# Kernel optimization log

Measured on AMD Instinct MI355X. Metric: run time of the kernel, lower is better.

Reference implementation:

```python
import jax, jax.numpy as jnp
import numpy as np
from jax import lax

_SQ2 = np.sqrt(2.0)
_H2 = (np.array([[1.0, 1.0], [1.0, -1.0]]) / _SQ2).astype(np.complex64)
_BN_INV = 1.0 / np.sqrt(1.0 + 1e-5)  # eval-mode BN, running_mean=0, running_var=1

# wire 0 is the most-significant bit of the 4-qubit basis index (PennyLane convention)
def _cnot_perm(c, t):
    p = np.arange(16)
    for b in range(16):
        if (b >> (3 - c)) & 1:
            p[b] = b ^ (1 << (3 - t))
    return p

# CNOT(0,1) then CNOT(1,2) then CNOT(2,3) then CNOT(3,0); psi_out = psi_in[perm]
_p01, _p12, _p23, _p30 = _cnot_perm(0, 1), _cnot_perm(1, 2), _cnot_perm(2, 3), _cnot_perm(3, 0)
_PTOT = _p01[_p12[_p23[_p30]]]
# PauliZ expectation signs: (16 basis states, 4 wires)
_ZM = np.array([[1.0 - 2.0 * ((b >> (3 - w)) & 1) for w in range(4)] for b in range(16)], np.float32)


def _make_unitaries(w0, w1):
    """w0, w1: (C,2). Circuit: H^4 -> RY(w0[0],w0[1],w0[0],w0[1]) -> RZ(w1 same pattern) -> CNOT ring."""
    ty = jnp.stack([w0[:, 0], w0[:, 1], w0[:, 0], w0[:, 1]], axis=1)  # (C,4)
    tz = jnp.stack([w1[:, 0], w1[:, 1], w1[:, 0], w1[:, 1]], axis=1)
    c, s = jnp.cos(ty / 2), jnp.sin(ty / 2)
    ry = jnp.stack([jnp.stack([c, -s], -1), jnp.stack([s, c], -1)], -2).astype(jnp.complex64)  # (C,4,2,2)
    ph = jnp.exp(-0.5j * tz.astype(jnp.complex64))  # (C,4)
    zr = jnp.zeros_like(ph)
    rz = jnp.stack([jnp.stack([ph, zr], -1), jnp.stack([zr, jnp.conj(ph)], -1)], -2)  # (C,4,2,2)
    g = rz @ ry @ jnp.asarray(_H2)  # per-wire single-qubit gate, (C,4,2,2)
    U = g[:, 0]
    for w in range(1, 4):  # kron over wires 0..3
        d = U.shape[1]
        U = jnp.einsum('cij,ckl->cikjl', U, g[:, w]).reshape(U.shape[0], d * 2, d * 2)
    return U[:, _PTOT, :]  # fold the CNOT-ring permutation into U


def _conv_bn_relu(x, w, g, b):
    y = lax.conv_general_dilated(x, w, (1, 1), ((1, 1), (1, 1)),
                                 dimension_numbers=('NCHW', 'OIHW', 'NCHW'))
    y = y * (g * _BN_INV)[None, :, None, None] + b[None, :, None, None]
    return jax.nn.relu(y)


def _bn_relu(x, g, b):
    return jax.nn.relu(x * (g * _BN_INV)[None, :, None, None] + b[None, :, None, None])


def _maxpool2(x):
    return lax.reduce_window(x, -jnp.inf, lax.max, (1, 1, 2, 2), (1, 1, 2, 2), 'VALID')


def _quantum_stage(e4, q_w0, q_w1):
    B, C, H, W = e4.shape
    xp = jnp.pad(e4, ((0, 0), (0, 0), (1, 2), (1, 2)))  # F.pad(1,2,1,2)
    # 4x4 patches, stride 1, row-major (matches torch unfold->view ordering): (B,C,H,W,16)
    patches = jnp.stack([xp[:, :, i:i + H, j:j + W] for i in range(4) for j in range(4)], axis=-1)
    nrm = jnp.sqrt(jnp.sum(patches * patches, axis=-1, keepdims=True))
    psi0 = (patches / jnp.maximum(nrm, 1e-12)).astype(jnp.complex64)  # AmplitudeEmbedding(normalize=True)
    U = _make_unitaries(q_w0, q_w1)  # (C,16,16) complex
    psi = jnp.einsum('cij,bchwj->bchwi', U, psi0)
    probs = psi.real ** 2 + psi.imag ** 2
    ev = jnp.einsum('bchwi,iq->bchwq', probs, jnp.asarray(_ZM))  # <Z_w> per wire
    return (ev.mean(-1) + 1.0) / 2.0


def setup_inputs() -> dict:
    key = jax.random.key(0)
    ks = jax.random.split(key, 18)
    conv_w = lambda k, o, i: jax.random.normal(k, (o, i, 3, 3), jnp.float32) / np.sqrt(i * 9)
    gamma = lambda k, c: jax.random.uniform(k, (c,), jnp.float32, 0.75, 1.25)
    beta = lambda k, c: 0.1 * jax.random.normal(k, (c,), jnp.float32)
    return {
        'x': jax.random.normal(ks[0], (8, 1, 256, 256), jnp.float32),
        'w1': conv_w(ks[1], 32, 1), 'g1': gamma(ks[2], 32), 'b1': beta(ks[3], 32),
        'w2': conv_w(ks[4], 64, 32), 'g2': gamma(ks[5], 64), 'b2': beta(ks[6], 64),
        'w3': conv_w(ks[7], 128, 64), 'g3': gamma(ks[8], 128), 'b3': beta(ks[9], 128),
        'w4': conv_w(ks[10], 256, 128), 'g4': gamma(ks[11], 256), 'b4': beta(ks[12], 256),
        'q_w0': 0.5 * jax.random.normal(ks[13], (256, 2), jnp.float32),
        'q_w1': 0.5 * jax.random.normal(ks[14], (256, 2), jnp.float32),
        'g5': gamma(ks[15], 256), 'b5': beta(ks[16], 256),
    }


def reference(x, w1, g1, b1, w2, g2, b2, w3, g3, b3, w4, g4, b4, q_w0, q_w1, g5, b5):
    e1 = _conv_bn_relu(x, w1, g1, b1)                 # (8,32,256,256)
    e2 = _conv_bn_relu(_maxpool2(e1), w2, g2, b2)     # (8,64,128,128)
    e3 = _conv_bn_relu(_maxpool2(e2), w3, g3, b3)     # (8,128,64,64)
    e4 = _conv_bn_relu(_maxpool2(e3), w4, g4, b4)     # (8,256,32,32)
    q = _quantum_stage(e4, q_w0, q_w1)                # (8,256,32,32)
    out4 = _bn_relu(q, g5, b5)
    return (e1, e2, e3, out4)
```

## Files before the change

kernel.cpp:

```cpp
#include <hip/hip_runtime.h>
#include <cstdint>
#include <cstddef>

#define BN_INV 0.9999950000374997f

typedef __attribute__((ext_vector_type(8))) _Float16 h8v;
typedef __attribute__((ext_vector_type(4))) float f4v;
typedef __attribute__((ext_vector_type(2))) float f2v;

__device__ __forceinline__ void fsplit(float v, ushort& h, ushort& l) {
    _Float16 hh = (_Float16)v;
    _Float16 ll = (_Float16)(v - (float)hh);
    h = __builtin_bit_cast(ushort, hh);
    l = __builtin_bit_cast(ushort, ll);
}

__device__ __forceinline__ void repack_one(
    const float* __restrict__ w, ushort* __restrict__ dst, int CIN, int i)
{
    int ocf = i / (CIN * 9);
    int r = i % (CIN * 9);
    int ic = r / 9;
    int tap = r % 9;
    int ocg = ocf >> 6, oc = ocf & 63;
    int chunk = ic >> 5, q = (ic >> 3) & 3, j = ic & 7;
    int nch = CIN >> 5;
    ushort h, l;
    fsplit(w[i], h, l);
    size_t base = (size_t)((ocg * nch + chunk) * 2) * 18432
                + (size_t)tap * 2048 + q * 512 + oc * 8 + j;
    dst[base] = h;
    dst[base + 18432] = l;
}

__global__ __launch_bounds__(256) void prep_conv1_kernel(
    const float* __restrict__ w0, const float* __restrict__ w1,
    float* __restrict__ U,
    const float* __restrict__ w2, ushort* __restrict__ wb2,
    const float* __restrict__ w3, ushort* __restrict__ wb3,
    const float* __restrict__ w4, ushort* __restrict__ wb4,
    const float* __restrict__ x, const float* __restrict__ wt,
    const float* __restrict__ g, const float* __restrict__ be,
    float* __restrict__ out, ushort* __restrict__ pooled)
{
    __shared__ float s_in[6][132];

    int blk = blockIdx.x;
    int tid = threadIdx.x;

    if (blk >= 1024) {
        if (blk >= 1400)     { repack_one(w4, wb4, 128, (blk - 1400) * 256 + tid); return; }
        if (blk >= 1112)     { repack_one(w3, wb3,  64, (blk - 1112) * 256 + tid); return; }
        if (blk >= 1040)     { repack_one(w2, wb2,  32, (blk - 1040) * 256 + tid); return; }

        int idx = (blk - 1024) * 256 + tid;
        int c = idx >> 4, r = idx & 15;
        float gr[4][2][2], gi[4][2][2];
        const float inv_sq2 = 0.70710678118654752f;
#pragma unroll
        for (int w = 0; w < 4; ++w) {
            float ty = w0[c * 2 + (w & 1)];
            float tz = w1[c * 2 + (w & 1)];
            float cy = cosf(0.5f * ty), sy = sinf(0.5f * ty);
            float cz = cosf(0.5f * tz), sz = sinf(0.5f * tz);
            float r00 = (cy - sy) * inv_sq2, r01 = (cy + sy) * inv_sq2;
            float r10 = (cy + sy) * inv_sq2, r11 = (sy - cy) * inv_sq2;
            gr[w][0][0] = cz * r00; gi[w][0][0] = -sz * r00;
            gr[w][0][1] = cz * r01; gi[w][0][1] = -sz * r01;
            gr[w][1][0] = cz * r10; gi[w][1][0] =  sz * r10;
            gr[w][1][1] = cz * r11; gi[w][1][1] =  sz * r11;
        }
        const int PTOT[16] = {0,13,3,14,6,11,5,8,12,1,15,2,10,7,9,4};
        int rp = PTOT[r];
        float* Uo = U + (size_t)c * 512 + r * 32;
#pragma unroll
        for (int cc = 0; cc < 16; ++cc) {
            float pr = 1.f, pi = 0.f;
#pragma unroll
            for (int w = 0; w < 4; ++w) {
                int ib = (rp >> (3 - w)) & 1, jb = (cc >> (3 - w)) & 1;
                float ar = gr[w][ib][jb], ai = gi[w][ib][jb];
                float nr = pr * ar - pi * ai;
                float ni = pr * ai + pi * ar;
                pr = nr; pi = ni;
            }
            Uo[cc * 2 + 0] = pr;
            Uo[cc * 2 + 1] = pi;
        }
        return;
    }

    int b = blk >> 7;
    int rest = blk & 127;
    int ty0 = (rest >> 1) * 4;
    int tx0 = (rest & 1) * 128;

    for (int i = tid; i < 780; i += 256) {
        int yy = i / 130, xx = i % 130;
        int gy = ty0 + yy - 1, gx = tx0 + xx - 1;
        float v = 0.f;
        if (gy >= 0 && gy < 256 && gx >= 0 && gx < 256)
            v = x[(size_t)b * 65536 + gy * 256 + gx];
        s_in[yy][xx] = v;
    }
    __syncthreads();

    int w = tid >> 6;
    int lane = tid & 63;
    int xp = (w & 1) * 32 + (lane >> 1);
    int ylo = lane & 1;
    int y = (w >> 1) * 2 + ylo;
    int x0s = xp * 2;

    f2v t2[3][3];
#pragma unroll
    for (int i = 0; i < 3; ++i) {
        f2v a = *(const f2v*)&s_in[y + i][x0s];
        f2v bq = *(const f2v*)&s_in[y + i][x0s + 2];
        t2[i][0] = a;
        t2[i][1] = (f2v){a.y, bq.x};
        t2[i][2] = bq;
    }

    bool wr_pool = (ylo == 0);
    int pyp = (ty0 >> 1) + (w >> 1);
    int pxp = (tx0 >> 1) + xp;
    ushort* op = pooled + (((size_t)b * 128 + pyp) * 128 + pxp) * 64;
    size_t obase = ((size_t)b * 32) * 65536 + (size_t)(ty0 + y) * 256 + (tx0 + x0s);

#pragma unroll
    for (int k = 0; k < 4; ++k) {
        uint uhw[4], ulw[4];
#pragma unroll
        for (int j2 = 0; j2 < 4; ++j2) {
            const int oc0 = k * 8 + j2 * 2;
            const int oc1 = oc0 + 1;
            f2v s0 = {0.f, 0.f}, s1 = {0.f, 0.f};
#pragma unroll
            for (int i = 0; i < 3; ++i)
#pragma unroll
                for (int j = 0; j < 3; ++j) {
                    s0 += wt[oc0 * 9 + i * 3 + j] * t2[i][j];
                    s1 += wt[oc1 * 9 + i * 3 + j] * t2[i][j];
                }
            float gs0 = g[oc0] * BN_INV, be0 = be[oc0];
            float gs1 = g[oc1] * BN_INV, be1 = be[oc1];
            s0 = s0 * gs0 + (f2v){be0, be0};
            s1 = s1 * gs1 + (f2v){be1, be1};
            s0.x = fmaxf(s0.x, 0.f); s0.y = fmaxf(s0.y, 0.f);
            s1.x = fmaxf(s1.x, 0.f); s1.y = fmaxf(s1.y, 0.f);
            *(f2v*)(out + obase + (size_t)oc0 * 65536) = s0;
            *(f2v*)(out + obase + (size_t)oc1 * 65536) = s1;
            float p0 = fmaxf(s0.x, s0.y);
            float p1 = fmaxf(s1.x, s1.y);
            p0 = fmaxf(p0, __shfl_xor(p0, 1));
            p1 = fmaxf(p1, __shfl_xor(p1, 1));
            auto hh = __builtin_amdgcn_cvt_pkrtz(p0, p1);
            uhw[j2] = __builtin_bit_cast(uint, hh);
            float l0 = p0 - (float)hh.x;
            float l1 = p1 - (float)hh.y;
            auto ll = __builtin_amdgcn_cvt_pkrtz(l0, l1);
            ulw[j2] = __builtin_bit_cast(uint, ll);
        }
        if (wr_pool) {
            uint4 uh = {uhw[0], uhw[1], uhw[2], uhw[3]};
            uint4 ul = {ulw[0], ulw[1], ulw[2], ulw[3]};
            *(uint4*)(op + 8 * k) = uh;
            *(uint4*)(op + 32 + 8 * k) = ul;
        }
    }
}

template <int CIN, int COUT, int HW, bool POOL>
__global__ __launch_bounds__(512) void conv3x3_mfma_split(
    const ushort* __restrict__ in,
    const ushort* __restrict__ wb,
    const float* __restrict__ g, const float* __restrict__ be,
    float* __restrict__ out,
    ushort* __restrict__ pooled)
{
    constexpr int NCH = CIN / 32;
    constexpr int NTX = HW / 16;
    constexpr int NT = NTX * (HW / 8);
    constexpr int NOCG = COUT / 64;
    constexpr int PS = 72;
    constexpr int BUFSZ = 180 * PS;
    constexpr int NBUF = (NCH > 1) ? 2 : 1;

    __shared__ __align__(16) ushort s_in[NBUF * BUFSZ];

    constexpr int NWG = NT * NOCG * 8;
    int bid = blockIdx.x;
    bid = (bid & 7) * (NWG >> 3) + (bid >> 3);

    int tile = bid % NT;
    int rest = bid / NT;
    int ocg = rest % NOCG;
    int b = rest / NOCG;
    int x0 = (tile % NTX) * 16;
    int y0 = (tile / NTX) * 8;

    int tid = threadIdx.x;
    int wv = tid >> 6;
    int lane = tid & 63;
    int n = lane & 15;
    int q = lane >> 4;
    int oc_half = (wv & 1) * 32;
    int sg = wv >> 1;

    int ib[2];
#pragma unroll
    for (int f = 0; f < 2; ++f)
        ib[f] = ((sg * 2 + f) * 18 + n) * PS + q * 8;
    int iwa0 = q * 512 + (oc_half + n) * 8;
    int iwa1 = q * 512 + (oc_half + 16 + n) * 8;

    const ushort* inb = in + (size_t)b * HW * HW * 2 * CIN;

    f4v acc[2][2];
#pragma unroll
    for (int a = 0; a < 2; ++a)
#pragma unroll
        for (int f = 0; f < 2; ++f) acc[a][f] = (f4v){0.f, 0.f, 0.f, 0.f};

    auto elem_addr = [&](int i, int& ldsoff, const ushort*& gsrc) {
        int pos = i >> 4;
        int r2 = i & 15;
        int comp = r2 >> 3;
        int u = r2 & 7;
        int py = pos / 18, px = pos % 18;
        int gy = y0 - 1 + py, gx = x0 - 1 + px;
        ldsoff = pos * PS + comp * 32 + u * 4;
        gsrc = (gy >= 0 && gy < HW && gx >= 0 && gx < HW)
             ? inb + ((size_t)gy * HW + gx) * (2 * CIN) + comp * CIN + u * 4
             : nullptr;
    };

#define TAPS(T0, T1)                                                             \
    _Pragma("unroll")                                                            \
    for (int tap = T0; tap < T1; ++tap) {                                        \
        const int toff = ((tap / 3) * 18 + (tap % 3)) * PS;                      \
        const ushort* wt_ = wc + tap * 2048;                                     \
        h8v ah0 = *(const h8v*)(wt_ + iwa0);                                     \
        h8v ah1 = *(const h8v*)(wt_ + iwa1);                                     \
        h8v al0 = *(const h8v*)(wt_ + 18432 + iwa0);                             \
        h8v al1 = *(const h8v*)(wt_ + 18432 + iwa1);                             \
        h8v bh[2], bl[2];                                                        \
        _Pragma("unroll")                                                        \
        for (int f = 0; f < 2; ++f) {                                            \
            bh[f] = *(const h8v*)(&sb[toff + ib[f]]);                            \
            bl[f] = *(const h8v*)(&sb[toff + ib[f] + 32]);                       \
        }                                                                        \
        _Pragma("unroll")                                                        \
        for (int f = 0; f < 2; ++f) {                                            \
            acc[0][f] = __builtin_amdgcn_mfma_f32_16x16x32_f16(ah0, bh[f], acc[0][f], 0, 0, 0); \
            acc[1][f] = __builtin_amdgcn_mfma_f32_16x16x32_f16(ah1, bh[f], acc[1][f], 0, 0, 0); \
        }                                                                        \
        _Pragma("unroll")                                                        \
        for (int f = 0; f < 2; ++f) {                                            \
            acc[0][f] = __builtin_amdgcn_mfma_f32_16x16x32_f16(ah0, bl[f], acc[0][f], 0, 0, 0); \
            acc[1][f] = __builtin_amdgcn_mfma_f32_16x16x32_f16(ah1, bl[f], acc[1][f], 0, 0, 0); \
        }                                                                        \
        _Pragma("unroll")                                                        \
        for (int f = 0; f < 2; ++f) {                                            \
            acc[0][f] = __builtin_amdgcn_mfma_f32_16x16x32_f16(al0, bh[f], acc[0][f], 0, 0, 0); \
            acc[1][f] = __builtin_amdgcn_mfma_f32_16x16x32_f16(al1, bh[f], acc[1][f], 0, 0, 0); \
        }                                                                        \
    }

    if constexpr (NCH == 1) {
#pragma unroll
        for (int it = 0; it < 5; ++it) {
            int i = tid + it * 512;
            if (i < 2304) {
                int lo; const ushort* src;
                elem_addr(i, lo, src);
                uint2 v; v.x = 0u; v.y = 0u;
                if (src) v = *(const uint2*)src;
                *(uint2*)(&s_in[lo]) = v;
            }
        }
        int lo0, lo1 = 0; const ushort* src0; const ushort* src1 = nullptr;
        elem_addr(2304 + tid, lo0, src0);
        bool has1 = tid < 64;
        if (has1) elem_addr(2816 + tid, lo1, src1);
        uint2 v0; v0.x = 0u; v0.y = 0u;
        uint2 v1; v1.x = 0u; v1.y = 0u;
        if (src0) v0 = *(const uint2*)src0;
        if (src1) v1 = *(const uint2*)src1;
        __syncthreads();

        const ushort* wc = wb + (size_t)(ocg * 2) * 18432;
        const ushort* sb = &s_in[0];
        __builtin_amdgcn_s_setprio(1);
        TAPS(0, 3)
        __builtin_amdgcn_s_setprio(0);
        *(uint2*)(&s_in[lo0]) = v0;
        if (has1) *(uint2*)(&s_in[lo1]) = v1;
        __syncthreads();
        __builtin_amdgcn_s_setprio(1);
        TAPS(3, 9)
        __builtin_amdgcn_s_setprio(0);
    } else {
        auto stage = [&](int ch, int bsel) {
#pragma unroll
            for (int it = 0; it < 6; ++it) {
                int i = tid + it * 512;
                if (i < 2880) {
                    int lo; const ushort* src;
                    elem_addr(i, lo, src);
                    uint2 v; v.x = 0u; v.y = 0u;
                    if (src) v = *(const uint2*)(src + (size_t)ch * 32);
                    *(uint2*)(&s_in[bsel * BUFSZ + lo]) = v;
                }
            }
        };

        stage(0, 0);
        int cur = 0;
        for (int ch = 0; ch < NCH; ++ch) {
            __syncthreads();
            if (ch + 1 < NCH) stage(ch + 1, cur ^ 1);

            const ushort* wc = wb + (size_t)((ocg * NCH + ch) * 2) * 18432;
            const ushort* sb = &s_in[cur * BUFSZ];
            __builtin_amdgcn_s_setprio(1);
            TAPS(0, 9)
            __builtin_amdgcn_s_setprio(0);
            cur ^= 1;
        }
    }
#undef TAPS

    float vr[2][2][4];
#pragma unroll
    for (int tf = 0; tf < 2; ++tf)
#pragma unroll
        for (int f = 0; f < 2; ++f) {
            int y = y0 + sg * 2 + f;
#pragma unroll
            for (int r = 0; r < 4; ++r) {
                int oc = ocg * 64 + oc_half + tf * 16 + q * 4 + r;
                float v = fmaxf(acc[tf][f][r] * (g[oc] * BN_INV) + be[oc], 0.f);
                vr[tf][f][r] = v;
                out[((size_t)(b * COUT + oc) * HW + y) * HW + (x0 + n)] = v;
            }
        }

    if (POOL) {
#pragma unroll
        for (int tf = 0; tf < 2; ++tf) {
            ushort h[4], l[4];
#pragma unroll
            for (int r = 0; r < 4; ++r) {
                float p = fmaxf(vr[tf][0][r], vr[tf][1][r]);
                p = fmaxf(p, __shfl_xor(p, 1));
                fsplit(p, h[r], l[r]);
            }
            if ((n & 1) == 0) {
                int pyp = (y0 >> 1) + sg;
                int pxp = (x0 + n) >> 1;
                int ocb = ocg * 64 + oc_half + tf * 16 + q * 4;
                ushort* op = pooled
                    + (((size_t)b * (HW / 2) + pyp) * (HW / 2) + pxp) * (2 * COUT);
                uint2 uh, ul;
                uh.x = (uint)h[0] | ((uint)h[1] << 16);
                uh.y = (uint)h[2] | ((uint)h[3] << 16);
                ul.x = (uint)l[0] | ((uint)l[1] << 16);
                ul.y = (uint)l[2] | ((uint)l[3] << 16);
                *(uint2*)(op + ocb) = uh;
                *(uint2*)(op + COUT + ocb) = ul;
            }
        }
    }
}

__global__ __launch_bounds__(256) void quantum_bn_relu(
    const float* __restrict__ e4,
    const float* __restrict__ U,
    const float* __restrict__ g5, const float* __restrict__ b5,
    float* __restrict__ out)
{
    int blk = blockIdx.x;
    int c = blk & 255;
    __shared__ float sp[35][36];
    __shared__ __align__(16) float sU[512];

    int tid = threadIdx.x;
    for (int i = tid; i < 35 * 36; i += 256) ((float*)sp)[i] = 0.f;
    const float4* Usrc = (const float4*)(U + (size_t)c * 512);
    if (tid < 128) ((float4*)sU)[tid] = Usrc[tid];
    float4 pv = ((const float4*)(e4 + (size_t)blk * 1024))[tid];
    __syncthreads();
    {
        int y = tid >> 3, x4 = (tid & 7) << 2;
        sp[y + 1][x4 + 1] = pv.x;
        sp[y + 1][x4 + 2] = pv.y;
        sp[y + 1][x4 + 3] = pv.z;
        sp[y + 1][x4 + 4] = pv.w;
    }
    __syncthreads();

    int y = tid >> 3, x4 = (tid & 7) << 2;
    float rows[4][8];
#pragma unroll
    for (int i = 0; i < 4; ++i) {
        float4 a = *(const float4*)&sp[y + i][x4];
        float4 bq = *(const float4*)&sp[y + i][x4 + 4];
        rows[i][0] = a.x;  rows[i][1] = a.y;  rows[i][2] = a.z;  rows[i][3] = a.w;
        rows[i][4] = bq.x; rows[i][5] = bq.y; rows[i][6] = bq.z; rows[i][7] = bq.w;
    }

    float inv2[4];
#pragma unroll
    for (int k = 0; k < 4; ++k) {
        float ss = 0.f;
#pragma unroll
        for (int i = 0; i < 4; ++i)
#pragma unroll
            for (int j = 0; j < 4; ++j) {
                float v = rows[i][k + j];
                ss += v * v;
            }
        float inv = 1.f / fmaxf(sqrtf(ss), 1e-12f);
        inv2[k] = inv * inv;
    }

    const int   RI[10] = {0, 1, 2, 4, 7, 8, 11, 13, 14, 15};
    const float ZM[10] = {1.f, .5f, .5f, .5f, -.5f, .5f, -.5f, -.5f, -.5f, -1.f};
    const float4* sU4 = (const float4*)sU;

    float s[4] = {0.f, 0.f, 0.f, 0.f};
#pragma unroll
    for (int ii = 0; ii < 10; ++ii) {
        int i = RI[ii];
        f2v p0 = {0.f, 0.f}, p1 = {0.f, 0.f}, p2 = {0.f, 0.f}, p3 = {0.f, 0.f};
#pragma unroll
        for (int jj = 0; jj < 8; ++jj) {
            float4 u = sU4[i * 8 + jj];
            f2v u01 = {u.x, u.y};
            f2v u23 = {u.z, u.w};
            const int e0 = 2 * jj, e1 = 2 * jj + 1;
            p0 += u01 * rows[e0 >> 2][0 + (e0 & 3)];
            p1 += u01 * rows[e0 >> 2][1 + (e0 & 3)];
            p2 += u01 * rows[e0 >> 2][2 + (e0 & 3)];
            p3 += u01 * rows[e0 >> 2][3 + (e0 & 3)];
            p0 += u23 * rows[e1 >> 2][0 + (e1 & 3)];
            p1 += u23 * rows[e1 >> 2][1 + (e1 & 3)];
            p2 += u23 * rows[e1 >> 2][2 + (e1 & 3)];
            p3 += u23 * rows[e1 >> 2][3 + (e1 & 3)];
        }
        float zm = ZM[ii];
        s[0] += (p0.x * p0.x + p0.y * p0.y) * zm;
        s[1] += (p1.x * p1.x + p1.y * p1.y) * zm;
        s[2] += (p2.x * p2.x + p2.y * p2.y) * zm;
        s[3] += (p3.x * p3.x + p3.y * p3.y) * zm;
    }

    float sc = g5[c] * BN_INV, bi = b5[c];
    float4 o;
    o.x = fmaxf(((s[0] * inv2[0] + 1.f) * 0.5f) * sc + bi, 0.f);
    o.y = fmaxf(((s[1] * inv2[1] + 1.f) * 0.5f) * sc + bi, 0.f);
    o.z = fmaxf(((s[2] * inv2[2] + 1.f) * 0.5f) * sc + bi, 0.f);
    o.w = fmaxf(((s[3] * inv2[3] + 1.f) * 0.5f) * sc + bi, 0.f);
    *(float4*)(out + (size_t)blk * 1024 + y * 32 + x4) = o;
}

extern "C" void kernel_launch(void* const* d_in, const int* in_sizes, int n_in,
                              void* d_out, int out_size, void* d_ws, size_t ws_size,
                              hipStream_t stream)
{
    const float* x   = (const float*)d_in[0];
    const float* w1  = (const float*)d_in[1];
    const float* g1  = (const float*)d_in[2];
    const float* b1  = (const float*)d_in[3];
    const float* w2  = (const float*)d_in[4];
    const float* g2  = (const float*)d_in[5];
    const float* b2  = (const float*)d_in[6];
    const float* w3  = (const float*)d_in[7];
    const float* g3  = (const float*)d_in[8];
    const float* b3  = (const float*)d_in[9];
    const float* w4  = (const float*)d_in[10];
    const float* g4  = (const float*)d_in[11];
    const float* b4  = (const float*)d_in[12];
    const float* qw0 = (const float*)d_in[13];
    const float* qw1 = (const float*)d_in[14];
    const float* g5  = (const float*)d_in[15];
    const float* b5  = (const float*)d_in[16];

    float* out = (float*)d_out;
    float* e1  = out;
    float* e2  = out + 16777216;
    float* e3  = out + 25165824;
    float* o4  = out + 29360128;

    float* ws = (float*)d_ws;
    float*  Uw  = ws;
    ushort* wb2 = (ushort*)(ws + 131072);
    ushort* wb3 = (ushort*)(ws + 149504);
    ushort* wb4 = (ushort*)(ws + 223232);
    ushort* pt1 = (ushort*)(ws + 518144);
    ushort* pt2 = (ushort*)(ws + 4712448);
    ushort* pt3 = (ushort*)(ws + 518144);

    prep_conv1_kernel<<<2552, 256, 0, stream>>>(
        qw0, qw1, Uw, w2, wb2, w3, wb3, w4, wb4,
        x, w1, g1, b1, e1, pt1);

    conv3x3_mfma_split<32, 64, 128, true><<<1024, 512, 0, stream>>>(pt1, wb2, g2, b2, e2, pt2);

    conv3x3_mfma_split<64, 128, 64, true><<<512, 512, 0, stream>>>(pt2, wb3, g3, b3, e3, pt3);

    conv3x3_mfma_split<128, 256, 32, false><<<256, 512, 0, stream>>>(pt3, wb4, g4, b4, o4, nullptr);

    quantum_bn_relu<<<2048, 256, 0, stream>>>(o4, Uw, g5, b5, o4);
}
```

Baseline: 242.7 us.

## Drop fp16 low-part split for activations, keep split only on weights

Activations passed between conv layers are now stored as a single fp16 value instead of a high/low fp16 pair, while weights still use the hi/lo split. This halves the pooled intermediate buffers, the global-to-LDS staging traffic and LDS footprint, and cuts the MFMA count per tap from six to four. In exchange the activation inputs lose their error-compensation term, so accuracy drops to roughly fp16 rounding on activations.

```diff
diff --git a/kernel.cpp b/kernel.cpp
--- a/kernel.cpp
+++ b/kernel.cpp
@@ -7,6 +7,11 @@
 typedef __attribute__((ext_vector_type(8))) _Float16 h8v;
 typedef __attribute__((ext_vector_type(4))) float f4v;
 typedef __attribute__((ext_vector_type(2))) float f2v;
+
+__device__ __forceinline__ ushort f16hi(float v) {
+    _Float16 hh = (_Float16)v;
+    return __builtin_bit_cast(ushort, hh);
+}
 
 __device__ __forceinline__ void fsplit(float v, ushort& h, ushort& l) {
     _Float16 hh = (_Float16)v;
@@ -125,12 +130,12 @@
     bool wr_pool = (ylo == 0);
     int pyp = (ty0 >> 1) + (w >> 1);
     int pxp = (tx0 >> 1) + xp;
-    ushort* op = pooled + (((size_t)b * 128 + pyp) * 128 + pxp) * 64;
+    ushort* op = pooled + (((size_t)b * 128 + pyp) * 128 + pxp) * 32;
     size_t obase = ((size_t)b * 32) * 65536 + (size_t)(ty0 + y) * 256 + (tx0 + x0s);
 
 #pragma unroll
     for (int k = 0; k < 4; ++k) {
-        uint uhw[4], ulw[4];
+        uint uhw[4];
 #pragma unroll
         for (int j2 = 0; j2 < 4; ++j2) {
             const int oc0 = k * 8 + j2 * 2;
@@ -155,24 +160,17 @@
             float p1 = fmaxf(s1.x, s1.y);
             p0 = fmaxf(p0, __shfl_xor(p0, 1));
             p1 = fmaxf(p1, __shfl_xor(p1, 1));
-            auto hh = __builtin_amdgcn_cvt_pkrtz(p0, p1);
-            uhw[j2] = __builtin_bit_cast(uint, hh);
-            float l0 = p0 - (float)hh.x;
-            float l1 = p1 - (float)hh.y;
-            auto ll = __builtin_amdgcn_cvt_pkrtz(l0, l1);
-            ulw[j2] = __builtin_bit_cast(uint, ll);
+            uhw[j2] = (uint)f16hi(p0) | ((uint)f16hi(p1) << 16);
         }
         if (wr_pool) {
             uint4 uh = {uhw[0], uhw[1], uhw[2], uhw[3]};
-            uint4 ul = {ulw[0], ulw[1], ulw[2], ulw[3]};
             *(uint4*)(op + 8 * k) = uh;
-            *(uint4*)(op + 32 + 8 * k) = ul;
         }
     }
 }
 
 template <int CIN, int COUT, int HW, bool POOL>
-__global__ __launch_bounds__(512) void conv3x3_mfma_split(
+__global__ __launch_bounds__(512) void conv3x3_mfma_wsplit(
     const ushort* __restrict__ in,
     const ushort* __restrict__ wb,
     const float* __restrict__ g, const float* __restrict__ be,
@@ -183,7 +181,7 @@
     constexpr int NTX = HW / 16;
     constexpr int NT = NTX * (HW / 8);
     constexpr int NOCG = COUT / 64;
-    constexpr int PS = 72;
+    constexpr int PS = 36;
     constexpr int BUFSZ = 180 * PS;
     constexpr int NBUF = (NCH > 1) ? 2 : 1;
 
@@ -215,7 +213,7 @@
     int iwa0 = q * 512 + (oc_half + n) * 8;
     int iwa1 = q * 512 + (oc_half + 16 + n) * 8;
 
-    const ushort* inb = in + (size_t)b * HW * HW * 2 * CIN;
+    const ushort* inb = in + (size_t)b * HW * HW * CIN;
 
     f4v acc[2][2];
 #pragma unroll
@@ -224,15 +222,13 @@
         for (int f = 0; f < 2; ++f) acc[a][f] = (f4v){0.f, 0.f, 0.f, 0.f};
 
     auto elem_addr = [&](int i, int& ldsoff, const ushort*& gsrc) {
-        int pos = i >> 4;
-        int r2 = i & 15;
-        int comp = r2 >> 3;
-        int u = r2 & 7;
+        int pos = i >> 3;
+        int u = i & 7;
         int py = pos / 18, px = pos % 18;
         int gy = y0 - 1 + py, gx = x0 - 1 + px;
-        ldsoff = pos * PS + comp * 32 + u * 4;
+        ldsoff = pos * PS + u * 4;
         gsrc = (gy >= 0 && gy < HW && gx >= 0 && gx < HW)
-             ? inb + ((size_t)gy * HW + gx) * (2 * CIN) + comp * CIN + u * 4
+             ? inb + ((size_t)gy * HW + gx) * CIN + u * 4
              : nullptr;
     };
 
@@ -245,12 +241,10 @@
         h8v ah1 = *(const h8v*)(wt_ + iwa1);                                     \
         h8v al0 = *(const h8v*)(wt_ + 18432 + iwa0);                             \
         h8v al1 = *(const h8v*)(wt_ + 18432 + iwa1);                             \
-        h8v bh[2], bl[2];                                                        \
+        h8v bh[2];                                                               \
         _Pragma("unroll")                                                        \
-        for (int f = 0; f < 2; ++f) {                                            \
+        for (int f = 0; f < 2; ++f)                                              \
             bh[f] = *(const h8v*)(&sb[toff + ib[f]]);                            \
-            bl[f] = *(const h8v*)(&sb[toff + ib[f] + 32]);                       \
-        }                                                                        \
         _Pragma("unroll")                                                        \
         for (int f = 0; f < 2; ++f) {                                            \
             acc[0][f] = __builtin_amdgcn_mfma_f32_16x16x32_f16(ah0, bh[f], acc[0][f], 0, 0, 0); \
@@ -258,11 +252,6 @@
         }                                                                        \
         _Pragma("unroll")                                                        \
         for (int f = 0; f < 2; ++f) {                                            \
-            acc[0][f] = __builtin_amdgcn_mfma_f32_16x16x32_f16(ah0, bl[f], acc[0][f], 0, 0, 0); \
-            acc[1][f] = __builtin_amdgcn_mfma_f32_16x16x32_f16(ah1, bl[f], acc[1][f], 0, 0, 0); \
-        }                                                                        \
-        _Pragma("unroll")                                                        \
-        for (int f = 0; f < 2; ++f) {                                            \
             acc[0][f] = __builtin_amdgcn_mfma_f32_16x16x32_f16(al0, bh[f], acc[0][f], 0, 0, 0); \
             acc[1][f] = __builtin_amdgcn_mfma_f32_16x16x32_f16(al1, bh[f], acc[1][f], 0, 0, 0); \
         }                                                                        \
@@ -270,9 +259,9 @@
 
     if constexpr (NCH == 1) {
 #pragma unroll
-        for (int it = 0; it < 5; ++it) {
+        for (int it = 0; it < 3; ++it) {
             int i = tid + it * 512;
-            if (i < 2304) {
+            if (i < 1152) {
                 int lo; const ushort* src;
                 elem_addr(i, lo, src);
                 uint2 v; v.x = 0u; v.y = 0u;
@@ -280,14 +269,11 @@
                 *(uint2*)(&s_in[lo]) = v;
             }
         }
-        int lo0, lo1 = 0; const ushort* src0; const ushort* src1 = nullptr;
-        elem_addr(2304 + tid, lo0, src0);
-        bool has1 = tid < 64;
-        if (has1) elem_addr(2816 + tid, lo1, src1);
+        bool has0 = tid < 288;
+        int lo0 = 0; const ushort* src0 = nullptr;
+        if (has0) elem_addr(1152 + tid, lo0, src0);
         uint2 v0; v0.x = 0u; v0.y = 0u;
-        uint2 v1; v1.x = 0u; v1.y = 0u;
         if (src0) v0 = *(const uint2*)src0;
-        if (src1) v1 = *(const uint2*)src1;
         __syncthreads();
 
         const ushort* wc = wb + (size_t)(ocg * 2) * 18432;
@@ -295,8 +281,7 @@
         __builtin_amdgcn_s_setprio(1);
         TAPS(0, 3)
         __builtin_amdgcn_s_setprio(0);
-        *(uint2*)(&s_in[lo0]) = v0;
-        if (has1) *(uint2*)(&s_in[lo1]) = v1;
+        if (has0) *(uint2*)(&s_in[lo0]) = v0;
         __syncthreads();
         __builtin_amdgcn_s_setprio(1);
         TAPS(3, 9)
@@ -304,9 +289,9 @@
     } else {
         auto stage = [&](int ch, int bsel) {
 #pragma unroll
-            for (int it = 0; it < 6; ++it) {
+            for (int it = 0; it < 3; ++it) {
                 int i = tid + it * 512;
-                if (i < 2880) {
+                if (i < 1440) {
                     int lo; const ushort* src;
                     elem_addr(i, lo, src);
                     uint2 v; v.x = 0u; v.y = 0u;
@@ -350,26 +335,23 @@
     if (POOL) {
 #pragma unroll
         for (int tf = 0; tf < 2; ++tf) {
-            ushort h[4], l[4];
+            ushort h[4];
 #pragma unroll
             for (int r = 0; r < 4; ++r) {
                 float p = fmaxf(vr[tf][0][r], vr[tf][1][r]);
                 p = fmaxf(p, __shfl_xor(p, 1));
-                fsplit(p, h[r], l[r]);
+                h[r] = f16hi(p);
             }
             if ((n & 1) == 0) {
                 int pyp = (y0 >> 1) + sg;
                 int pxp = (x0 + n) >> 1;
                 int ocb = ocg * 64 + oc_half + tf * 16 + q * 4;
                 ushort* op = pooled
-                    + (((size_t)b * (HW / 2) + pyp) * (HW / 2) + pxp) * (2 * COUT);
-                uint2 uh, ul;
+                    + (((size_t)b * (HW / 2) + pyp) * (HW / 2) + pxp) * COUT;
+                uint2 uh;
                 uh.x = (uint)h[0] | ((uint)h[1] << 16);
                 uh.y = (uint)h[2] | ((uint)h[3] << 16);
-                ul.x = (uint)l[0] | ((uint)l[1] << 16);
-                ul.y = (uint)l[2] | ((uint)l[3] << 16);
                 *(uint2*)(op + ocb) = uh;
-                *(uint2*)(op + COUT + ocb) = ul;
             }
         }
     }
@@ -500,18 +482,18 @@
     ushort* wb3 = (ushort*)(ws + 149504);
     ushort* wb4 = (ushort*)(ws + 223232);
     ushort* pt1 = (ushort*)(ws + 518144);
-    ushort* pt2 = (ushort*)(ws + 4712448);
+    ushort* pt2 = (ushort*)(ws + 2615296);
     ushort* pt3 = (ushort*)(ws + 518144);
 
     prep_conv1_kernel<<<2552, 256, 0, stream>>>(
         qw0, qw1, Uw, w2, wb2, w3, wb3, w4, wb4,
         x, w1, g1, b1, e1, pt1);
 
-    conv3x3_mfma_split<32, 64, 128, true><<<1024, 512, 0, stream>>>(pt1, wb2, g2, b2, e2, pt2);
-
-    conv3x3_mfma_split<64, 128, 64, true><<<512, 512, 0, stream>>>(pt2, wb3, g3, b3, e3, pt3);
-
-    conv3x3_mfma_split<128, 256, 32, false><<<256, 512, 0, stream>>>(pt3, wb4, g4, b4, o4, nullptr);
+    conv3x3_mfma_wsplit<32, 64, 128, true><<<1024, 512, 0, stream>>>(pt1, wb2, g2, b2, e2, pt2);
+
+    conv3x3_mfma_wsplit<64, 128, 64, true><<<512, 512, 0, stream>>>(pt2, wb3, g3, b3, e3, pt3);
+
+    conv3x3_mfma_wsplit<128, 256, 32, false><<<256, 512, 0, stream>>>(pt3, wb4, g4, b4, o4, nullptr);
 
     quantum_bn_relu<<<2048, 256, 0, stream>>>(o4, Uw, g5, b5, o4);
 }
```

Measured after the change: 247.6 us. 2.0% more time.
